# Kernel optimization log

Hardware: AMD Instinct MI355X
Metric: run time of the kernel (lower is better)

## Reference

```python
import jax, jax.numpy as jnp
import numpy as np

N_NODES = 8192
N_EDGES = 262144
N_VIEWS = 2


def setup_inputs() -> dict:
    key = jax.random.key(0)
    k1, k2, k3, k4, k5, k6 = jax.random.split(key, 6)
    x = jax.random.normal(k1, (N_NODES, 512), dtype=jnp.float32)
    # Glorot-ish scaling for GCN weights
    W1 = jax.random.normal(k2, (512, 256), dtype=jnp.float32) * (1.0 / np.sqrt(512))
    W2 = jax.random.normal(k3, (256, 128), dtype=jnp.float32) * (1.0 / np.sqrt(256))
    edge_vals = jax.random.uniform(k4, (N_EDGES,), dtype=jnp.float32)
    edge_rows = jax.random.randint(k5, (N_EDGES,), 0, N_NODES, dtype=jnp.int32)
    edge_cols = jax.random.randint(k6, (N_EDGES,), 0, N_NODES, dtype=jnp.int32)
    return {"x": x, "W1": W1, "W2": W2, "edge_vals": edge_vals,
            "edge_rows": edge_rows, "edge_cols": edge_cols}


def reference(x, W1, W2, edge_vals, edge_rows, edge_cols):
    # GraphConvolution: support = x @ W ; out = spmm(adj, support) ; act (relu, dropout=0)
    def spmm(h):
        # out[i] = sum_e A[rows[e], cols[e]] * h[cols[e]]  -- irregular gather + segment reduce
        return jax.ops.segment_sum(edge_vals[:, None] * h[edge_cols], edge_rows,
                                   num_segments=N_NODES)

    # Forward quirk in the source: every view uses adjs[0], and mean over n_views
    # identical embeddings == a single pass, so one spmm per layer is exact.
    h = jax.nn.relu(spmm(x @ W1))        # [N, 256]
    z = jax.nn.relu(spmm(h @ W2))        # [N, 128]  (self.embeddings)

    # InnerProductDecoder with act = identity (lambda x: x from Model_2 default)
    rec = z @ z.T                         # [N, N]
    rec_views = jnp.stack([rec] * N_VIEWS, axis=0)  # n_views identical decoders
    return z, rec_views
```

## Files before the change

### kernel.cpp

```cpp
#include <hip/hip_runtime.h>

#define NN 8192
#define NE 262144

typedef short bf16x8 __attribute__((ext_vector_type(8)));
typedef float f32x16 __attribute__((ext_vector_type(16)));
typedef float f32x4 __attribute__((ext_vector_type(4)));

__device__ __forceinline__ unsigned short f2bf(float f) {
  unsigned u = __float_as_uint(f);
  u += 0x7fffu + ((u >> 16) & 1u);
  return (unsigned short)(u >> 16);
}
__device__ __forceinline__ float bflo(unsigned u) { return __uint_as_float(u << 16); }
__device__ __forceinline__ float bfhi(unsigned u) { return __uint_as_float(u & 0xffff0000u); }

__global__ void k_prep(const float* __restrict__ x, const float* __restrict__ W1,
                       const float* __restrict__ W2, unsigned short* __restrict__ xb,
                       unsigned short* __restrict__ W1t, unsigned short* __restrict__ W2t,
                       int* __restrict__ counts) {
  int id = blockIdx.x * blockDim.x + threadIdx.x;
  int stride = gridDim.x * blockDim.x;
  for (int t = id; t < (NN * 512) / 4; t += stride) {
    float4 v = *(const float4*)(x + (size_t)t * 4);
    unsigned lo = (unsigned)f2bf(v.x) | ((unsigned)f2bf(v.y) << 16);
    unsigned hi = (unsigned)f2bf(v.z) | ((unsigned)f2bf(v.w) << 16);
    *(uint2*)(xb + (size_t)t * 4) = make_uint2(lo, hi);
  }
  for (int t = id; t < 512 * 256; t += stride) {
    int k = t >> 8, c = t & 255;
    W1t[c * 512 + k] = f2bf(W1[t]);
  }
  for (int t = id; t < 256 * 128; t += stride) {
    int k = t >> 7, c = t & 127;
    W2t[c * 256 + k] = f2bf(W2[t]);
  }
  for (int t = id; t < NN; t += stride) counts[t] = 0;
}

__global__ void k_hist(const int* __restrict__ rows, int* __restrict__ counts) {
  int id = blockIdx.x * blockDim.x + threadIdx.x;
  if (id < NE) atomicAdd(&counts[rows[id]], 1);
}

__global__ void k_scan(const int* __restrict__ counts, int* __restrict__ starts,
                       int* __restrict__ cursor) {
  __shared__ int sums[1024];
  int t = threadIdx.x;
  int base = t * 8;
  int local[8];
  int s = 0;
  #pragma unroll
  for (int i = 0; i < 8; ++i) { local[i] = s; s += counts[base + i]; }
  sums[t] = s;
  __syncthreads();
  for (int off = 1; off < 1024; off <<= 1) {
    int v = 0;
    if (t >= off) v = sums[t - off];
    __syncthreads();
    sums[t] += v;
    __syncthreads();
  }
  int pre = sums[t] - s;
  #pragma unroll
  for (int i = 0; i < 8; ++i) {
    starts[base + i] = pre + local[i];
    cursor[base + i] = pre + local[i];
  }
  if (t == 1023) starts[NN] = sums[1023];
}

__global__ void k_scatter(const int* __restrict__ rows, const float* __restrict__ vals,
                          const int* __restrict__ cols, int* __restrict__ cursor,
                          float* __restrict__ ev_s, int* __restrict__ ec_s) {
  int id = blockIdx.x * blockDim.x + threadIdx.x;
  if (id < NE) {
    int pos = atomicAdd(&cursor[rows[id]], 1);
    ev_s[pos] = vals[id];
    ec_s[pos] = cols[id];
  }
}

template <int K, int N>
__global__ __launch_bounds__(256) void k_gemm(const unsigned short* __restrict__ Ab,
                                              const unsigned short* __restrict__ Bt,
                                              unsigned short* __restrict__ Cb) {
  __shared__ unsigned char As[128 * 64 * 2];
  __shared__ unsigned char Bs[64 * 64 * 2];
  const int tid = threadIdx.x;
  const int r0 = blockIdx.x * 128, c0 = blockIdx.y * 64;
  const int wid = tid >> 6, lane = tid & 63;
  const int wrow = wid >> 1, wcol = wid & 1;
  const int lr = lane & 31, lg = lane >> 5;

  f32x16 acc[2] = {};

  for (int kc = 0; kc < K; kc += 64) {
    __syncthreads();
    for (int q = tid; q < 1024; q += 256) {
      int r = q >> 3, s = q & 7;
      float4 v = *(const float4*)(Ab + (size_t)(r0 + r) * K + kc + s * 8);
      *(float4*)(As + r * 128 + ((s * 16) ^ ((r & 7) << 4))) = v;
    }
    for (int q = tid; q < 512; q += 256) {
      int r = q >> 3, s = q & 7;
      float4 v = *(const float4*)(Bt + (size_t)(c0 + r) * K + kc + s * 8);
      *(float4*)(Bs + r * 128 + ((s * 16) ^ ((r & 7) << 4))) = v;
    }
    __syncthreads();
    #pragma unroll
    for (int ks = 0; ks < 4; ++ks) {
      int brow = wcol * 32 + lr;
      bf16x8 bf = *(const bf16x8*)(Bs + brow * 128 + ((ks * 32 + lg * 16) ^ ((brow & 7) << 4)));
      #pragma unroll
      for (int m = 0; m < 2; ++m) {
        int arow = wrow * 64 + m * 32 + lr;
        bf16x8 af = *(const bf16x8*)(As + arow * 128 + ((ks * 32 + lg * 16) ^ ((arow & 7) << 4)));
        acc[m] = __builtin_amdgcn_mfma_f32_32x32x16_bf16(bf, af, acc[m], 0, 0, 0);
      }
    }
  }
  #pragma unroll
  for (int m = 0; m < 2; ++m) {
    int row = r0 + wrow * 64 + m * 32 + lr;
    #pragma unroll
    for (int g = 0; g < 4; ++g) {
      unsigned lo = (unsigned)f2bf(acc[m][4 * g + 0]) | ((unsigned)f2bf(acc[m][4 * g + 1]) << 16);
      unsigned hi = (unsigned)f2bf(acc[m][4 * g + 2]) | ((unsigned)f2bf(acc[m][4 * g + 3]) << 16);
      int colc = c0 + wcol * 32 + 8 * g + 4 * lg;
      *(uint2*)(Cb + (size_t)row * N + colc) = make_uint2(lo, hi);
    }
  }
}

template <int F>
__global__ __launch_bounds__(256) void k_spmm(const int* __restrict__ starts,
                                              const float* __restrict__ ev_s,
                                              const int* __restrict__ ec_s,
                                              const unsigned short* __restrict__ Sb,
                                              float* __restrict__ outF,
                                              unsigned short* __restrict__ outB) {
  constexpr int V = F / 64;
  int gw = (blockIdx.x * blockDim.x + threadIdx.x) >> 6;
  int lane = threadIdx.x & 63;
  if (gw >= NN) return;
  int s = starts[gw], e = starts[gw + 1];
  float acc[V];
  #pragma unroll
  for (int v = 0; v < V; ++v) acc[v] = 0.f;
  for (int j = s; j < e; ++j) {
    float w = ev_s[j];
    int c = ec_s[j];
    if constexpr (V == 4) {
      uint2 t = *(const uint2*)(Sb + (size_t)c * F + lane * 4);
      acc[0] += w * bflo(t.x); acc[1] += w * bfhi(t.x);
      acc[2] += w * bflo(t.y); acc[3] += w * bfhi(t.y);
    } else {
      unsigned t = *(const unsigned*)(Sb + (size_t)c * F + lane * 2);
      acc[0] += w * bflo(t); acc[1] += w * bfhi(t);
    }
  }
  #pragma unroll
  for (int v = 0; v < V; ++v) acc[v] = fmaxf(acc[v], 0.f);
  if constexpr (V == 4) {
    unsigned lo = (unsigned)f2bf(acc[0]) | ((unsigned)f2bf(acc[1]) << 16);
    unsigned hi = (unsigned)f2bf(acc[2]) | ((unsigned)f2bf(acc[3]) << 16);
    *(uint2*)(outB + (size_t)gw * F + lane * 4) = make_uint2(lo, hi);
  } else {
    unsigned lo = (unsigned)f2bf(acc[0]) | ((unsigned)f2bf(acc[1]) << 16);
    *(unsigned int*)(outB + (size_t)gw * F + lane * 2) = lo;
    if (outF) {
      *(float2*)(outF + (size_t)gw * F + lane * 2) = make_float2(acc[0], acc[1]);
    }
  }
}

__global__ __launch_bounds__(256) void k_rec(const unsigned short* __restrict__ zb,
                                             float* __restrict__ out0,
                                             float* __restrict__ out1) {
  __shared__ unsigned char lds[49152];
  unsigned char* Ai = lds;
  unsigned char* Bj = lds + 16384;
  const int tid = threadIdx.x;
  const int i0 = blockIdx.x * 64, j0 = blockIdx.y * 128;

  for (int q = tid; q < 1024; q += 256) {
    int r = q >> 4, s = q & 15;
    float4 v = *(const float4*)(zb + (size_t)(i0 + r) * 128 + s * 8);
    *(float4*)(Ai + r * 256 + ((s * 16) ^ ((r & 15) << 4))) = v;
  }
  for (int q = tid; q < 2048; q += 256) {
    int r = q >> 4, s = q & 15;
    float4 v = *(const float4*)(zb + (size_t)(j0 + r) * 128 + s * 8);
    *(float4*)(Bj + r * 256 + ((s * 16) ^ ((r & 15) << 4))) = v;
  }
  __syncthreads();

  const int wid = tid >> 6, lane = tid & 63;
  const int wrow = wid >> 1, wcol = wid & 1;
  const int lr = lane & 31, lg = lane >> 5;

  f32x16 acc[2] = {};
  #pragma unroll
  for (int ks = 0; ks < 8; ++ks) {
    int arow = wrow * 32 + lr;
    bf16x8 af = *(const bf16x8*)(Ai + arow * 256 + ((ks * 32 + lg * 16) ^ ((arow & 15) << 4)));
    #pragma unroll
    for (int m = 0; m < 2; ++m) {
      int brow = wcol * 64 + m * 32 + lr;
      bf16x8 bf = *(const bf16x8*)(Bj + brow * 256 + ((ks * 32 + lg * 16) ^ ((brow & 15) << 4)));
      acc[m] = __builtin_amdgcn_mfma_f32_32x32x16_bf16(bf, af, acc[m], 0, 0, 0);
    }
  }

  __syncthreads();
  float* T = (float*)lds;
  {
    int row = wrow * 32 + lr;
    #pragma unroll
    for (int m = 0; m < 2; ++m) {
      #pragma unroll
      for (int q = 0; q < 4; ++q) {
        int col = wcol * 64 + m * 32 + 8 * q + 4 * lg;
        f32x4 v = {acc[m][4 * q + 0], acc[m][4 * q + 1], acc[m][4 * q + 2], acc[m][4 * q + 3]};
        *(f32x4*)(T + row * 132 + col) = v;
      }
    }
  }
  __syncthreads();
  {
    int rr = tid >> 5, cc = (tid & 31) * 4;
    #pragma unroll
    for (int p = 0; p < 8; ++p) {
      int row = p * 8 + rr;
      f32x4 v = *(const f32x4*)(T + row * 132 + cc);
      size_t idx = (size_t)(i0 + row) * NN + (size_t)(j0 + cc);
      __builtin_nontemporal_store(v, (f32x4*)(out0 + idx));
      __builtin_nontemporal_store(v, (f32x4*)(out1 + idx));
    }
  }
}

extern "C" void kernel_launch(void* const* d_in, const int* in_sizes, int n_in,
                              void* d_out, int out_size, void* d_ws, size_t ws_size,
                              hipStream_t stream) {
  const float* x     = (const float*)d_in[0];
  const float* W1    = (const float*)d_in[1];
  const float* W2    = (const float*)d_in[2];
  const float* evals = (const float*)d_in[3];
  const int*   erows = (const int*)d_in[4];
  const int*   ecols = (const int*)d_in[5];

  float* out_z   = (float*)d_out;
  float* out_r0  = out_z + (size_t)NN * 128;
  float* out_r1  = out_r0 + (size_t)NN * NN;

  char* w = (char*)d_ws;
  unsigned short* W1t = (unsigned short*)w;  w += 256 * 512 * 2;
  unsigned short* W2t = (unsigned short*)w;  w += 128 * 256 * 2;
  unsigned short* xb  = (unsigned short*)w;  w += (size_t)NN * 512 * 2;
  unsigned short* g1  = (unsigned short*)w;  w += (size_t)NN * 256 * 2;
  unsigned short* h1  = (unsigned short*)w;  w += (size_t)NN * 256 * 2;
  unsigned short* g2  = (unsigned short*)w;  w += (size_t)NN * 128 * 2;
  unsigned short* zb  = (unsigned short*)w;  w += (size_t)NN * 128 * 2;
  int*   counts = (int*)w;                   w += NN * 4;
  int*   starts = (int*)w;                   w += (NN + 8) * 4;
  int*   cursor = (int*)w;                   w += NN * 4;
  float* ev_s   = (float*)w;                 w += NE * 4;
  int*   ec_s   = (int*)w;                   w += NE * 4;

  k_prep<<<256, 256, 0, stream>>>(x, W1, W2, xb, W1t, W2t, counts);
  k_hist<<<NE / 256, 256, 0, stream>>>(erows, counts);
  k_scan<<<1, 1024, 0, stream>>>(counts, starts, cursor);
  k_scatter<<<NE / 256, 256, 0, stream>>>(erows, evals, ecols, cursor, ev_s, ec_s);

  k_gemm<512, 256><<<dim3(64, 4), 256, 0, stream>>>(xb, W1t, g1);
  k_spmm<256><<<NN / 4, 256, 0, stream>>>(starts, ev_s, ec_s, g1, nullptr, h1);
  k_gemm<256, 128><<<dim3(64, 2), 256, 0, stream>>>(h1, W2t, g2);
  k_spmm<128><<<NN / 4, 256, 0, stream>>>(starts, ev_s, ec_s, g2, out_z, zb);
  k_rec<<<dim3(128, 64), 256, 0, stream>>>(zb, out_r0, out_r1);
}
```

Before: 701.2 us.

## Use 512-thread GEMM blocks, swap rec grid order, drop nontemporal stores

```diff
diff --git a/kernel.cpp b/kernel.cpp
--- a/kernel.cpp
+++ b/kernel.cpp
@@ -82,7 +82,7 @@
 }
 
 template <int K, int N>
-__global__ __launch_bounds__(256) void k_gemm(const unsigned short* __restrict__ Ab,
+__global__ __launch_bounds__(512) void k_gemm(const unsigned short* __restrict__ Ab,
                                               const unsigned short* __restrict__ Bt,
                                               unsigned short* __restrict__ Cb) {
   __shared__ unsigned char As[128 * 64 * 2];
@@ -90,44 +90,44 @@
   const int tid = threadIdx.x;
   const int r0 = blockIdx.x * 128, c0 = blockIdx.y * 64;
   const int wid = tid >> 6, lane = tid & 63;
-  const int wrow = wid >> 1, wcol = wid & 1;
+  const int wr = wid >> 1, wc = wid & 1;
   const int lr = lane & 31, lg = lane >> 5;
 
-  f32x16 acc[2] = {};
+  f32x16 acc = {};
 
   for (int kc = 0; kc < K; kc += 64) {
     __syncthreads();
-    for (int q = tid; q < 1024; q += 256) {
+    #pragma unroll
+    for (int q = tid; q < 1024; q += 512) {
       int r = q >> 3, s = q & 7;
       float4 v = *(const float4*)(Ab + (size_t)(r0 + r) * K + kc + s * 8);
       *(float4*)(As + r * 128 + ((s * 16) ^ ((r & 7) << 4))) = v;
     }
-    for (int q = tid; q < 512; q += 256) {
-      int r = q >> 3, s = q & 7;
-      float4 v = *(const float4*)(Bt + (size_t)(c0 + r) * K + kc + s * 8);
-      *(float4*)(Bs + r * 128 + ((s * 16) ^ ((r & 7) << 4))) = v;
+    {
+      int q = tid;
+      if (q < 512) {
+        int r = q >> 3, s = q & 7;
+        float4 v = *(const float4*)(Bt + (size_t)(c0 + r) * K + kc + s * 8);
+        *(float4*)(Bs + r * 128 + ((s * 16) ^ ((r & 7) << 4))) = v;
+      }
     }
     __syncthreads();
     #pragma unroll
     for (int ks = 0; ks < 4; ++ks) {
-      int brow = wcol * 32 + lr;
+      int brow = wc * 32 + lr;
       bf16x8 bf = *(const bf16x8*)(Bs + brow * 128 + ((ks * 32 + lg * 16) ^ ((brow & 7) << 4)));
-      #pragma unroll
-      for (int m = 0; m < 2; ++m) {
-        int arow = wrow * 64 + m * 32 + lr;
-        bf16x8 af = *(const bf16x8*)(As + arow * 128 + ((ks * 32 + lg * 16) ^ ((arow & 7) << 4)));
-        acc[m] = __builtin_amdgcn_mfma_f32_32x32x16_bf16(bf, af, acc[m], 0, 0, 0);
-      }
-    }
-  }
-  #pragma unroll
-  for (int m = 0; m < 2; ++m) {
-    int row = r0 + wrow * 64 + m * 32 + lr;
+      int arow = wr * 32 + lr;
+      bf16x8 af = *(const bf16x8*)(As + arow * 128 + ((ks * 32 + lg * 16) ^ ((arow & 7) << 4)));
+      acc = __builtin_amdgcn_mfma_f32_32x32x16_bf16(bf, af, acc, 0, 0, 0);
+    }
+  }
+  {
+    int row = r0 + wr * 32 + lr;
     #pragma unroll
     for (int g = 0; g < 4; ++g) {
-      unsigned lo = (unsigned)f2bf(acc[m][4 * g + 0]) | ((unsigned)f2bf(acc[m][4 * g + 1]) << 16);
-      unsigned hi = (unsigned)f2bf(acc[m][4 * g + 2]) | ((unsigned)f2bf(acc[m][4 * g + 3]) << 16);
-      int colc = c0 + wcol * 32 + 8 * g + 4 * lg;
+      unsigned lo = (unsigned)f2bf(acc[4 * g + 0]) | ((unsigned)f2bf(acc[4 * g + 1]) << 16);
+      unsigned hi = (unsigned)f2bf(acc[4 * g + 2]) | ((unsigned)f2bf(acc[4 * g + 3]) << 16);
+      int colc = c0 + wc * 32 + 8 * g + 4 * lg;
       *(uint2*)(Cb + (size_t)row * N + colc) = make_uint2(lo, hi);
     }
   }
@@ -182,7 +182,7 @@
   unsigned char* Ai = lds;
   unsigned char* Bj = lds + 16384;
   const int tid = threadIdx.x;
-  const int i0 = blockIdx.x * 64, j0 = blockIdx.y * 128;
+  const int i0 = blockIdx.y * 64, j0 = blockIdx.x * 128;
 
   for (int q = tid; q < 1024; q += 256) {
     int r = q >> 4, s = q & 15;
@@ -235,8 +235,8 @@
       int row = p * 8 + rr;
       f32x4 v = *(const f32x4*)(T + row * 132 + cc);
       size_t idx = (size_t)(i0 + row) * NN + (size_t)(j0 + cc);
-      __builtin_nontemporal_store(v, (f32x4*)(out0 + idx));
-      __builtin_nontemporal_store(v, (f32x4*)(out1 + idx));
+      *(f32x4*)(out0 + idx) = v;
+      *(f32x4*)(out1 + idx) = v;
     }
   }
 }
@@ -274,9 +274,9 @@
   k_scan<<<1, 1024, 0, stream>>>(counts, starts, cursor);
   k_scatter<<<NE / 256, 256, 0, stream>>>(erows, evals, ecols, cursor, ev_s, ec_s);
 
-  k_gemm<512, 256><<<dim3(64, 4), 256, 0, stream>>>(xb, W1t, g1);
+  k_gemm<512, 256><<<dim3(64, 4), 512, 0, stream>>>(xb, W1t, g1);
   k_spmm<256><<<NN / 4, 256, 0, stream>>>(starts, ev_s, ec_s, g1, nullptr, h1);
-  k_gemm<256, 128><<<dim3(64, 2), 256, 0, stream>>>(h1, W2t, g2);
+  k_gemm<256, 128><<<dim3(64, 2), 512, 0, stream>>>(h1, W2t, g2);
   k_spmm<128><<<NN / 4, 256, 0, stream>>>(starts, ev_s, ec_s, g2, out_z, zb);
-  k_rec<<<dim3(128, 64), 256, 0, stream>>>(zb, out_r0, out_r1);
-}
+  k_rec<<<dim3(64, 128), 256, 0, stream>>>(zb, out_r0, out_r1);
+}
```

New measurement: 653.2 us. 1.07x faster.
